# Performance work log

Hardware: AMD Instinct MI355X
Metric: run time of the kernel (lower is better)

## Reference

```python
import jax, jax.numpy as jnp
import numpy as np

N_NODES = 50000
N_EDGES = 800000
NEG_SLOPE = 0.2  # leaky_relu slope used in the model


def setup_inputs() -> dict:
    key = jax.random.key(0)
    ks = jax.random.split(key, 8)
    d_in, d_h, d_out = 64, 64, 4
    x = jax.random.normal(ks[0], (N_NODES, d_in), dtype=jnp.float32)
    edge_index = jax.random.randint(ks[1], (2, N_EDGES), 0, N_NODES, dtype=jnp.int32)
    # Glorot-style init like PyG GCNConv
    W0 = jax.random.normal(ks[2], (d_in, d_h), dtype=jnp.float32) * np.float32(1.0 / np.sqrt(d_in))
    W1 = jax.random.normal(ks[3], (d_h, d_h), dtype=jnp.float32) * np.float32(1.0 / np.sqrt(d_h))
    W2 = jax.random.normal(ks[4], (d_h, d_out), dtype=jnp.float32) * np.float32(1.0 / np.sqrt(d_h))
    b0 = jnp.zeros((d_h,), dtype=jnp.float32)
    b1 = jnp.zeros((d_h,), dtype=jnp.float32)
    b2 = jnp.zeros((d_out,), dtype=jnp.float32)
    return {"x": x, "edge_index": edge_index, "W0": W0, "b0": b0,
            "W1": W1, "b1": b1, "W2": W2, "b2": b2}


def _gcn_norm(edge_index, n_nodes, dtype):
    # Add self-loops, compute symmetric normalization D^{-1/2} (A+I) D^{-1/2}
    src, dst = edge_index[0], edge_index[1]
    loop = jnp.arange(n_nodes, dtype=src.dtype)
    src = jnp.concatenate([src, loop])
    dst = jnp.concatenate([dst, loop])
    deg = jax.ops.segment_sum(jnp.ones_like(dst, dtype=dtype), dst, num_segments=n_nodes)
    dinv = jnp.where(deg > 0, jax.lax.rsqrt(deg), jnp.zeros_like(deg))
    norm = dinv[src] * dinv[dst]  # [E + N]
    return src, dst, norm


def _gcn_layer(h, src, dst, norm, W, b, n_nodes):
    h = h @ W                                  # [N, d_out]
    msg = h[src] * norm[:, None]               # gather + edge scaling
    out = jax.ops.segment_sum(msg, dst, num_segments=n_nodes)  # scatter-add
    return out + b


def reference(x, edge_index, W0, b0, W1, b1, W2, b2):
    # Eval-mode forward: dropout_edge and F.dropout are identity when not training.
    n = x.shape[0]
    src, dst, norm = _gcn_norm(edge_index, n, x.dtype)
    h = _gcn_layer(x, src, dst, norm, W0, b0, n)
    h = jax.nn.leaky_relu(h, NEG_SLOPE)
    h = _gcn_layer(h, src, dst, norm, W1, b1, n)
    h = jax.nn.leaky_relu(h, NEG_SLOPE)
    out = _gcn_layer(h, src, dst, norm, W2, b2, n)
    return out
```

## Files before the change

kernel.cpp:

```cpp
#include <hip/hip_runtime.h>
#include <math.h>

#define NEG_SLOPE 0.2f
#define NPAD 50176
#define NW8  (NPAD / 4)
#define NCHUNK 128

typedef _Float16 half4 __attribute__((ext_vector_type(4)));

__global__ __launch_bounds__(1024) void k_hist(const int* __restrict__ dst,
                                               unsigned int* __restrict__ histw,
                                               int e, int es) {
    extern __shared__ unsigned int lcnt[];
    int t = threadIdx.x;
    for (int w = t; w < NW8; w += 1024) lcnt[w] = 0u;
    __syncthreads();
    int beg = blockIdx.x * es;
    int end = min(beg + es, e);
    for (int i = beg + t; i < end; i += 1024) {
        int d = dst[i];
        atomicAdd(&lcnt[d >> 2], 1u << ((d & 3) << 3));
    }
    __syncthreads();
    unsigned int* out = histw + (size_t)blockIdx.x * NW8;
    for (int w = t; w < NW8; w += 1024) out[w] = lcnt[w];
}

__global__ __launch_bounds__(256) void k_chscan(unsigned char* __restrict__ hist8,
                                                float* __restrict__ dinv,
                                                unsigned short* __restrict__ deg16,
                                                int* __restrict__ bsum, int n) {
    int t = threadIdx.x;
    int i = blockIdx.x * 256 + t;
    unsigned char* p = hist8 + i;
    unsigned int run = 0;
    for (int c = 0; c < NCHUNK; c += 8) {
        size_t b = (size_t)c * NPAD;
        unsigned char v0 = p[b];
        unsigned char v1 = p[b + (size_t)1 * NPAD];
        unsigned char v2 = p[b + (size_t)2 * NPAD];
        unsigned char v3 = p[b + (size_t)3 * NPAD];
        unsigned char v4 = p[b + (size_t)4 * NPAD];
        unsigned char v5 = p[b + (size_t)5 * NPAD];
        unsigned char v6 = p[b + (size_t)6 * NPAD];
        unsigned char v7 = p[b + (size_t)7 * NPAD];
        unsigned int e0 = run;
        unsigned int e1 = e0 + v0;
        unsigned int e2 = e1 + v1;
        unsigned int e3 = e2 + v2;
        unsigned int e4 = e3 + v3;
        unsigned int e5 = e4 + v4;
        unsigned int e6 = e5 + v5;
        unsigned int e7 = e6 + v6;
        run = e7 + v7;
        p[b] = (unsigned char)e0;
        p[b + (size_t)1 * NPAD] = (unsigned char)e1;
        p[b + (size_t)2 * NPAD] = (unsigned char)e2;
        p[b + (size_t)3 * NPAD] = (unsigned char)e3;
        p[b + (size_t)4 * NPAD] = (unsigned char)e4;
        p[b + (size_t)5 * NPAD] = (unsigned char)e5;
        p[b + (size_t)6 * NPAD] = (unsigned char)e6;
        p[b + (size_t)7 * NPAD] = (unsigned char)e7;
    }
    int deg = (int)run;
    if (i < n) dinv[i] = rsqrtf((float)(deg + 1));
    deg16[i] = (unsigned short)deg;
    int s = deg;
    for (int d = 1; d < 64; d <<= 1) s += __shfl_down(s, d);
    __shared__ int ws[4];
    if ((t & 63) == 0) ws[t >> 6] = s;
    __syncthreads();
    if (t == 0) bsum[blockIdx.x] = ws[0] + ws[1] + ws[2] + ws[3];
}

__global__ __launch_bounds__(256) void k_scan3(const unsigned short* __restrict__ deg16,
                                               const int* __restrict__ bsum,
                                               int* __restrict__ rowptr, int n, int nb) {
    __shared__ int ls[256];
    __shared__ int wo[4];
    int t = threadIdx.x;
    int bid = blockIdx.x;
    int bv = (t < bid && t < nb) ? bsum[t] : 0;
    for (int d = 1; d < 64; d <<= 1) bv += __shfl_down(bv, d);
    if ((t & 63) == 0) wo[t >> 6] = bv;
    __syncthreads();
    int boff = wo[0] + wo[1] + wo[2] + wo[3];
    int i = bid * 256 + t;
    int v = (i < n) ? (int)deg16[i] : 0;
    ls[t] = v;
    __syncthreads();
    for (int d = 1; d < 256; d <<= 1) {
        int u = (t >= d) ? ls[t - d] : 0;
        __syncthreads();
        ls[t] += u;
        __syncthreads();
    }
    int excl = ls[t] - v + boff;
    if (i < n) rowptr[i] = excl;
    if (i == n - 1) rowptr[n] = excl + v;
}

__global__ __launch_bounds__(1024) void k_place2(const int* __restrict__ src,
                                                 const int* __restrict__ dst,
                                                 const int* __restrict__ rowptr,
                                                 const unsigned int* __restrict__ choffw,
                                                 int* __restrict__ perm, int e, int es) {
    extern __shared__ unsigned int cur[];
    int t = threadIdx.x;
    const unsigned int* in = choffw + (size_t)blockIdx.x * NW8;
    for (int w = t; w < NW8; w += 1024) cur[w] = in[w];
    __syncthreads();
    int beg = blockIdx.x * es;
    int end = min(beg + es, e);
    for (int i = beg + t; i < end; i += 1024) {
        int d = dst[i];
        int sh = (d & 3) << 3;
        unsigned int old = atomicAdd(&cur[d >> 2], 1u << sh);
        int slot = rowptr[d] + (int)((old >> sh) & 0xffu);
        perm[slot] = src[i];
    }
}

template <typename T>
__global__ __launch_bounds__(256) void k_gemm64(const T* __restrict__ in,
                                                const float* __restrict__ W,
                                                const float* __restrict__ dinv,
                                                _Float16* __restrict__ out, int n) {
    __shared__ float Ws[64 * 64];
    __shared__ float Xs[16 * 64];
    int t = threadIdx.x;
    const float4* W4 = (const float4*)W;
    float4* Ws4 = (float4*)Ws;
#pragma unroll
    for (int i = 0; i < 4; ++i) Ws4[t + 256 * i] = W4[t + 256 * i];
    int row0 = blockIdx.x * 16;
    {
        int r = t >> 4, c4 = t & 15;
        int row = row0 + r;
        float4 v = make_float4(0.f, 0.f, 0.f, 0.f);
        if (row < n) {
            if constexpr (sizeof(T) == 4) {
                v = ((const float4*)(in + (size_t)row * 64))[c4];
            } else {
                half4 hv = ((const half4*)(in + (size_t)row * 64))[c4];
                v = make_float4((float)hv.x, (float)hv.y, (float)hv.z, (float)hv.w);
            }
        }
        ((float4*)Xs)[t] = v;
    }
    __syncthreads();
    int c = t & 63, g = t >> 6;
    float a0 = 0.f, a1 = 0.f, a2 = 0.f, a3 = 0.f;
#pragma unroll
    for (int k = 0; k < 64; ++k) {
        float w = Ws[k * 64 + c];
        a0 = fmaf(Xs[g * 64 + k], w, a0);
        a1 = fmaf(Xs[(g + 4) * 64 + k], w, a1);
        a2 = fmaf(Xs[(g + 8) * 64 + k], w, a2);
        a3 = fmaf(Xs[(g + 12) * 64 + k], w, a3);
    }
    int r;
    r = row0 + g;      if (r < n) out[(size_t)r * 64 + c] = (_Float16)(a0 * dinv[r]);
    r = row0 + g + 4;  if (r < n) out[(size_t)r * 64 + c] = (_Float16)(a1 * dinv[r]);
    r = row0 + g + 8;  if (r < n) out[(size_t)r * 64 + c] = (_Float16)(a2 * dinv[r]);
    r = row0 + g + 12; if (r < n) out[(size_t)r * 64 + c] = (_Float16)(a3 * dinv[r]);
}

__global__ __launch_bounds__(256) void k_gather64(
        const _Float16* __restrict__ h, const float* __restrict__ dinv,
        const int* __restrict__ rowptr, const int* __restrict__ perm,
        const float* __restrict__ b, _Float16* __restrict__ out, int n, int act,
        const float* __restrict__ W2, float* __restrict__ y, int fuse) {
    int t = threadIdx.x;
    int v = blockIdx.x * 4 + (t >> 6);
    if (v >= n) return;
    v = __builtin_amdgcn_readfirstlane(v);
    int lane = t & 63;
    const _Float16* hl = h + lane;
    float acc = (float)hl[(size_t)v * 64];
    int e = rowptr[v], end = rowptr[v + 1];
#define LOADK(j) float x##j = (float)hl[(size_t)perm[e + j] * 64]
    for (; e + 16 <= end; e += 16) {
        LOADK(0); LOADK(1); LOADK(2); LOADK(3);
        LOADK(4); LOADK(5); LOADK(6); LOADK(7);
        LOADK(8); LOADK(9); LOADK(10); LOADK(11);
        LOADK(12); LOADK(13); LOADK(14); LOADK(15);
        acc += (((x0 + x1) + (x2 + x3)) + ((x4 + x5) + (x6 + x7)))
             + (((x8 + x9) + (x10 + x11)) + ((x12 + x13) + (x14 + x15)));
    }
    if (e + 8 <= end) {
        LOADK(0); LOADK(1); LOADK(2); LOADK(3);
        LOADK(4); LOADK(5); LOADK(6); LOADK(7);
        acc += ((x0 + x1) + (x2 + x3)) + ((x4 + x5) + (x6 + x7));
        e += 8;
    }
    if (e + 4 <= end) {
        LOADK(0); LOADK(1); LOADK(2); LOADK(3);
        acc += (x0 + x1) + (x2 + x3);
        e += 4;
    }
    if (e + 2 <= end) {
        LOADK(0); LOADK(1);
        acc += x0 + x1;
        e += 2;
    }
    if (e < end) acc += (float)hl[(size_t)perm[e] * 64];
#undef LOADK
    float dv = dinv[v];
    acc = acc * dv + b[lane];
    if (act) acc = acc > 0.0f ? acc : acc * NEG_SLOPE;
    if (!fuse) {
        out[(size_t)v * 64 + lane] = (_Float16)acc;
    } else {
        float4 w = ((const float4*)W2)[lane];
        float p0 = acc * w.x, p1 = acc * w.y, p2 = acc * w.z, p3 = acc * w.w;
#pragma unroll
        for (int dlt = 1; dlt < 64; dlt <<= 1) {
            p0 += __shfl_xor(p0, dlt);
            p1 += __shfl_xor(p1, dlt);
            p2 += __shfl_xor(p2, dlt);
            p3 += __shfl_xor(p3, dlt);
        }
        if (lane == 0)
            ((float4*)y)[v] = make_float4(p0 * dv, p1 * dv, p2 * dv, p3 * dv);
    }
}

__global__ __launch_bounds__(256) void k_gather4(
        const float* __restrict__ h, const float* __restrict__ dinv,
        const int* __restrict__ rowptr, const int* __restrict__ perm,
        const float* __restrict__ b, float* __restrict__ out, int n) {
    int gid = blockIdx.x * 256 + threadIdx.x;
    int c = gid & 3;
    int v = gid >> 2;
    if (v >= n) return;
    const float* hc = h + c;
    float acc = hc[(size_t)v * 4];
    int e = rowptr[v], end = rowptr[v + 1];
    for (; e + 4 <= end; e += 4) {
        float x0 = hc[(size_t)perm[e] * 4];
        float x1 = hc[(size_t)perm[e + 1] * 4];
        float x2 = hc[(size_t)perm[e + 2] * 4];
        float x3 = hc[(size_t)perm[e + 3] * 4];
        acc += (x0 + x1) + (x2 + x3);
    }
    for (; e < end; ++e) acc += hc[(size_t)perm[e] * 4];
    out[(size_t)v * 4 + c] = acc * dinv[v] + b[c];
}

extern "C" void kernel_launch(void* const* d_in, const int* in_sizes, int n_in,
                              void* d_out, int out_size, void* d_ws, size_t ws_size,
                              hipStream_t stream) {
    const float* x  = (const float*)d_in[0];
    const int* ei   = (const int*)d_in[1];
    const float* W0 = (const float*)d_in[2];
    const float* b0 = (const float*)d_in[3];
    const float* W1 = (const float*)d_in[4];
    const float* b1 = (const float*)d_in[5];
    const float* W2 = (const float*)d_in[6];
    const float* b2 = (const float*)d_in[7];
    float* out = (float*)d_out;

    const int N = in_sizes[0] / 64;
    const int E = in_sizes[1] / 2;
    const int* src = ei;
    const int* dst = ei + E;
    const int es = (E + NCHUNK - 1) / NCHUNK;

    char* base = (char*)d_ws;
    size_t off = 0;
    auto alloc = [&](size_t bytes) { size_t o = off; off = (off + bytes + 255) & ~(size_t)255; return o; };
    unsigned int*   histw  = (unsigned int*)(base + alloc((size_t)NCHUNK * NPAD));
    unsigned short* deg16  = (unsigned short*)(base + alloc((size_t)NPAD * 2));
    float*          dinv   = (float*)(base + alloc((size_t)NPAD * 4));
    int*            rowptr = (int*)(base + alloc((size_t)(NPAD + 1) * 4));
    int*            bsum   = (int*)(base + alloc(1024));
    int*            perm   = (int*)(base + alloc((size_t)E * 4));
    _Float16*       bufH   = (_Float16*)(base + alloc((size_t)N * 64 * 2));
    _Float16*       bufB16 = (_Float16*)(base + alloc((size_t)N * 64 * 2));
    float*          bufD   = (float*)(base + alloc((size_t)N * 4 * 4));

    const int nb_N = (N + 255) / 256;
    const int nb_V = (N + 3) / 4;

    k_hist<<<NCHUNK, 1024, NW8 * sizeof(unsigned int), stream>>>(dst, histw, E, es);
    k_chscan<<<NPAD / 256, 256, 0, stream>>>((unsigned char*)histw, dinv, deg16, bsum, N);
    k_scan3<<<nb_N, 256, 0, stream>>>(deg16, bsum, rowptr, N, nb_N);
    k_place2<<<NCHUNK, 1024, NW8 * sizeof(unsigned int), stream>>>(src, dst, rowptr, histw, perm, E, es);

    k_gemm64<float><<<(N + 15) / 16, 256, 0, stream>>>(x, W0, dinv, bufH, N);
    k_gather64<<<nb_V, 256, 0, stream>>>(bufH, dinv, rowptr, perm, b0, bufB16, N, 1,
                                         W2, bufD, 0);

    k_gemm64<_Float16><<<(N + 15) / 16, 256, 0, stream>>>(bufB16, W1, dinv, bufH, N);
    k_gather64<<<nb_V, 256, 0, stream>>>(bufH, dinv, rowptr, perm, b1, bufB16, N, 1,
                                         W2, bufD, 1);

    k_gather4<<<(N * 4 + 255) / 256, 256, 0, stream>>>(bufD, dinv, rowptr, perm, b2, out, N);
}
```

Baseline: 159.3 us.

## Fuse CSR build kernels into one cooperative kernel with grid syncs

Merges the histogram, per-chunk scan, row-pointer scan and edge placement kernels into a single cooperative launch of 128 blocks that uses grid.sync between phases. The goal is to remove three kernel launch boundaries and their gaps. In exchange, the scan phases now run on only 128 blocks of 1024 threads, and the block-offset prefix is a serial loop in thread 0. Launching cooperatively adds its own overhead, and it needs all 128 blocks resident at once with about 50KB of LDS each.

```diff
diff --git a/kernel.cpp b/kernel.cpp
--- a/kernel.cpp
+++ b/kernel.cpp
@@ -1,5 +1,8 @@
 #include <hip/hip_runtime.h>
+#include <hip/hip_cooperative_groups.h>
 #include <math.h>
+
+namespace cg = cooperative_groups;
 
 #define NEG_SLOPE 0.2f
 #define NPAD 50176
@@ -8,116 +11,116 @@
 
 typedef _Float16 half4 __attribute__((ext_vector_type(4)));
 
-__global__ __launch_bounds__(1024) void k_hist(const int* __restrict__ dst,
-                                               unsigned int* __restrict__ histw,
-                                               int e, int es) {
-    extern __shared__ unsigned int lcnt[];
+__global__ void k_csr(const int* __restrict__ dst, const int* __restrict__ src,
+                      unsigned int* __restrict__ histw, float* __restrict__ dinv,
+                      unsigned short* __restrict__ deg16, int* __restrict__ bsum,
+                      int* __restrict__ rowptr, int* __restrict__ perm,
+                      int e, int es, int n) {
+    extern __shared__ unsigned int sbuf[];
+    int* ls = (int*)(sbuf + NW8);
+    __shared__ int ws2[20];
+    cg::grid_group grid = cg::this_grid();
     int t = threadIdx.x;
-    for (int w = t; w < NW8; w += 1024) lcnt[w] = 0u;
+    int b = blockIdx.x;
+
+    for (int w = t; w < NW8; w += 1024) sbuf[w] = 0u;
     __syncthreads();
-    int beg = blockIdx.x * es;
+    int beg = b * es;
     int end = min(beg + es, e);
     for (int i = beg + t; i < end; i += 1024) {
         int d = dst[i];
-        atomicAdd(&lcnt[d >> 2], 1u << ((d & 3) << 3));
+        atomicAdd(&sbuf[d >> 2], 1u << ((d & 3) << 3));
     }
     __syncthreads();
-    unsigned int* out = histw + (size_t)blockIdx.x * NW8;
-    for (int w = t; w < NW8; w += 1024) out[w] = lcnt[w];
-}
-
-__global__ __launch_bounds__(256) void k_chscan(unsigned char* __restrict__ hist8,
-                                                float* __restrict__ dinv,
-                                                unsigned short* __restrict__ deg16,
-                                                int* __restrict__ bsum, int n) {
-    int t = threadIdx.x;
-    int i = blockIdx.x * 256 + t;
-    unsigned char* p = hist8 + i;
-    unsigned int run = 0;
-    for (int c = 0; c < NCHUNK; c += 8) {
-        size_t b = (size_t)c * NPAD;
-        unsigned char v0 = p[b];
-        unsigned char v1 = p[b + (size_t)1 * NPAD];
-        unsigned char v2 = p[b + (size_t)2 * NPAD];
-        unsigned char v3 = p[b + (size_t)3 * NPAD];
-        unsigned char v4 = p[b + (size_t)4 * NPAD];
-        unsigned char v5 = p[b + (size_t)5 * NPAD];
-        unsigned char v6 = p[b + (size_t)6 * NPAD];
-        unsigned char v7 = p[b + (size_t)7 * NPAD];
-        unsigned int e0 = run;
-        unsigned int e1 = e0 + v0;
-        unsigned int e2 = e1 + v1;
-        unsigned int e3 = e2 + v2;
-        unsigned int e4 = e3 + v3;
-        unsigned int e5 = e4 + v4;
-        unsigned int e6 = e5 + v5;
-        unsigned int e7 = e6 + v6;
-        run = e7 + v7;
-        p[b] = (unsigned char)e0;
-        p[b + (size_t)1 * NPAD] = (unsigned char)e1;
-        p[b + (size_t)2 * NPAD] = (unsigned char)e2;
-        p[b + (size_t)3 * NPAD] = (unsigned char)e3;
-        p[b + (size_t)4 * NPAD] = (unsigned char)e4;
-        p[b + (size_t)5 * NPAD] = (unsigned char)e5;
-        p[b + (size_t)6 * NPAD] = (unsigned char)e6;
-        p[b + (size_t)7 * NPAD] = (unsigned char)e7;
-    }
-    int deg = (int)run;
-    if (i < n) dinv[i] = rsqrtf((float)(deg + 1));
-    deg16[i] = (unsigned short)deg;
-    int s = deg;
-    for (int d = 1; d < 64; d <<= 1) s += __shfl_down(s, d);
-    __shared__ int ws[4];
-    if ((t & 63) == 0) ws[t >> 6] = s;
+    {
+        unsigned int* out = histw + (size_t)b * NW8;
+        for (int w = t; w < NW8; w += 1024) out[w] = sbuf[w];
+    }
+    grid.sync();
+
+    int i2 = b * 1024 + t;
+    int deg = 0;
+    if (i2 < NPAD) {
+        unsigned char* p = (unsigned char*)histw + i2;
+        unsigned int run = 0;
+        for (int c = 0; c < NCHUNK; c += 8) {
+            size_t bb = (size_t)c * NPAD;
+            unsigned char v0 = p[bb];
+            unsigned char v1 = p[bb + (size_t)1 * NPAD];
+            unsigned char v2 = p[bb + (size_t)2 * NPAD];
+            unsigned char v3 = p[bb + (size_t)3 * NPAD];
+            unsigned char v4 = p[bb + (size_t)4 * NPAD];
+            unsigned char v5 = p[bb + (size_t)5 * NPAD];
+            unsigned char v6 = p[bb + (size_t)6 * NPAD];
+            unsigned char v7 = p[bb + (size_t)7 * NPAD];
+            unsigned int e0 = run;
+            unsigned int e1 = e0 + v0;
+            unsigned int e2 = e1 + v1;
+            unsigned int e3 = e2 + v2;
+            unsigned int e4 = e3 + v3;
+            unsigned int e5 = e4 + v4;
+            unsigned int e6 = e5 + v5;
+            unsigned int e7 = e6 + v6;
+            run = e7 + v7;
+            p[bb] = (unsigned char)e0;
+            p[bb + (size_t)1 * NPAD] = (unsigned char)e1;
+            p[bb + (size_t)2 * NPAD] = (unsigned char)e2;
+            p[bb + (size_t)3 * NPAD] = (unsigned char)e3;
+            p[bb + (size_t)4 * NPAD] = (unsigned char)e4;
+            p[bb + (size_t)5 * NPAD] = (unsigned char)e5;
+            p[bb + (size_t)6 * NPAD] = (unsigned char)e6;
+            p[bb + (size_t)7 * NPAD] = (unsigned char)e7;
+        }
+        deg = (int)run;
+        if (i2 < n) dinv[i2] = rsqrtf((float)(deg + 1));
+        deg16[i2] = (unsigned short)deg;
+    }
+    {
+        int s = deg;
+        for (int d = 1; d < 64; d <<= 1) s += __shfl_down(s, d);
+        __syncthreads();
+        if ((t & 63) == 0) ls[t >> 6] = s;
+        __syncthreads();
+        if (t == 0) {
+            int s16 = 0;
+            for (int w = 0; w < 16; ++w) s16 += ls[w];
+            bsum[b] = s16;
+        }
+    }
+    grid.sync();
+
+    if (t == 0) {
+        int s = 0;
+        for (int j = 0; j < b; ++j) s += bsum[j];
+        ws2[0] = s;
+    }
+    int v3 = (i2 < n) ? (int)deg16[i2] : 0;
+    ls[t] = v3;
     __syncthreads();
-    if (t == 0) bsum[blockIdx.x] = ws[0] + ws[1] + ws[2] + ws[3];
-}
-
-__global__ __launch_bounds__(256) void k_scan3(const unsigned short* __restrict__ deg16,
-                                               const int* __restrict__ bsum,
-                                               int* __restrict__ rowptr, int n, int nb) {
-    __shared__ int ls[256];
-    __shared__ int wo[4];
-    int t = threadIdx.x;
-    int bid = blockIdx.x;
-    int bv = (t < bid && t < nb) ? bsum[t] : 0;
-    for (int d = 1; d < 64; d <<= 1) bv += __shfl_down(bv, d);
-    if ((t & 63) == 0) wo[t >> 6] = bv;
-    __syncthreads();
-    int boff = wo[0] + wo[1] + wo[2] + wo[3];
-    int i = bid * 256 + t;
-    int v = (i < n) ? (int)deg16[i] : 0;
-    ls[t] = v;
-    __syncthreads();
-    for (int d = 1; d < 256; d <<= 1) {
+    for (int d = 1; d < 1024; d <<= 1) {
         int u = (t >= d) ? ls[t - d] : 0;
         __syncthreads();
         ls[t] += u;
         __syncthreads();
     }
-    int excl = ls[t] - v + boff;
-    if (i < n) rowptr[i] = excl;
-    if (i == n - 1) rowptr[n] = excl + v;
-}
-
-__global__ __launch_bounds__(1024) void k_place2(const int* __restrict__ src,
-                                                 const int* __restrict__ dst,
-                                                 const int* __restrict__ rowptr,
-                                                 const unsigned int* __restrict__ choffw,
-                                                 int* __restrict__ perm, int e, int es) {
-    extern __shared__ unsigned int cur[];
-    int t = threadIdx.x;
-    const unsigned int* in = choffw + (size_t)blockIdx.x * NW8;
-    for (int w = t; w < NW8; w += 1024) cur[w] = in[w];
-    __syncthreads();
-    int beg = blockIdx.x * es;
-    int end = min(beg + es, e);
-    for (int i = beg + t; i < end; i += 1024) {
-        int d = dst[i];
-        int sh = (d & 3) << 3;
-        unsigned int old = atomicAdd(&cur[d >> 2], 1u << sh);
-        int slot = rowptr[d] + (int)((old >> sh) & 0xffu);
-        perm[slot] = src[i];
+    {
+        int excl = ls[t] - v3 + ws2[0];
+        if (i2 < n) rowptr[i2] = excl;
+        if (i2 == n - 1) rowptr[n] = excl + v3;
+    }
+    grid.sync();
+
+    {
+        const unsigned int* in = histw + (size_t)b * NW8;
+        for (int w = t; w < NW8; w += 1024) sbuf[w] = in[w];
+        __syncthreads();
+        for (int i = beg + t; i < end; i += 1024) {
+            int d = dst[i];
+            int sh = (d & 3) << 3;
+            unsigned int old = atomicAdd(&sbuf[d >> 2], 1u << sh);
+            int slot = rowptr[d] + (int)((old >> sh) & 0xffu);
+            perm[slot] = src[i];
+        }
     }
 }
 
@@ -280,13 +283,25 @@
     _Float16*       bufB16 = (_Float16*)(base + alloc((size_t)N * 64 * 2));
     float*          bufD   = (float*)(base + alloc((size_t)N * 4 * 4));
 
-    const int nb_N = (N + 255) / 256;
     const int nb_V = (N + 3) / 4;
 
-    k_hist<<<NCHUNK, 1024, NW8 * sizeof(unsigned int), stream>>>(dst, histw, E, es);
-    k_chscan<<<NPAD / 256, 256, 0, stream>>>((unsigned char*)histw, dinv, deg16, bsum, N);
-    k_scan3<<<nb_N, 256, 0, stream>>>(deg16, bsum, rowptr, N, nb_N);
-    k_place2<<<NCHUNK, 1024, NW8 * sizeof(unsigned int), stream>>>(src, dst, rowptr, histw, perm, E, es);
+    {
+        int e_ = E, es_ = es, n_ = N;
+        const int* dst_ = dst;
+        const int* src_ = src;
+        unsigned int* histw_ = histw;
+        float* dinv_ = dinv;
+        unsigned short* deg16_ = deg16;
+        int* bsum_ = bsum;
+        int* rowptr_ = rowptr;
+        int* perm_ = perm;
+        void* args[] = {(void*)&dst_, (void*)&src_, (void*)&histw_, (void*)&dinv_,
+                        (void*)&deg16_, (void*)&bsum_, (void*)&rowptr_, (void*)&perm_,
+                        (void*)&e_, (void*)&es_, (void*)&n_};
+        size_t shmem = (size_t)(NW8 + 1024) * sizeof(unsigned int);
+        hipLaunchCooperativeKernel((void*)k_csr, dim3(NCHUNK), dim3(1024),
+                                   args, (unsigned int)shmem, stream);
+    }
 
     k_gemm64<float><<<(N + 15) / 16, 256, 0, stream>>>(x, W0, dinv, bufH, N);
     k_gather64<<<nb_V, 256, 0, stream>>>(bufH, dinv, rowptr, perm, b0, bufB16, N, 1,
```

Measured after the change: 226.2 us. 42.0% more time.
